# Performance work log

Measured on AMD Instinct MI355X. Metric: run time of the kernel, lower is better.

The kernel has to match this reference:

```python
import jax, jax.numpy as jnp
import numpy as np

N, IN_DIM, OUT_DIM, H = 8192, 128, 128, 2
HD = OUT_DIM // H
NEG_SLOPE = 0.2


def setup_inputs() -> dict:
    key = jax.random.key(0)
    k1, k2, k3, k4, k5 = jax.random.split(key, 5)
    x = jax.random.normal(k1, (N, IN_DIM), dtype=jnp.float32)
    adj = jax.random.randint(k2, (N, N), 0, 2).astype(jnp.float32)
    W = jax.random.normal(k3, (IN_DIM, OUT_DIM), dtype=jnp.float32) / np.sqrt(IN_DIM)
    a_src = jax.random.normal(k4, (H, HD), dtype=jnp.float32) * 0.01
    a_dst = jax.random.normal(k5, (H, HD), dtype=jnp.float32) * 0.01
    return {"x": x, "adj": adj, "W": W, "a_src": a_src, "a_dst": a_dst}


def reference(x, adj, W, a_src, a_dst):
    # h: (N, H, HD)
    h = (x @ W).reshape(N, H, HD)
    # per-node additive score halves: (N, H)
    e_src = jnp.einsum('nhd,hd->nh', h, a_src)
    e_dst = jnp.einsum('nhd,hd->nh', h, a_dst)
    # attn logits: (N_i, N_j, H); torch code adds e_src[i] + e_dst[j]
    logits = jax.nn.leaky_relu(e_src[:, None, :] + e_dst[None, :, :], NEG_SLOPE)
    logits = jnp.where(adj[:, :, None] > 0, logits, -jnp.inf)
    # softmax over neighbor axis j (dim=1), matching F.softmax(attn, dim=1)
    attn = jax.nn.softmax(logits, axis=1)
    # dropout omitted (eval mode)
    out = jnp.einsum('ijh,jhd->ihd', attn, h).reshape(N, OUT_DIM)
    return out
```

## Files before the change

kernel.cpp:

```cpp
#include <hip/hip_runtime.h>
#include <hip/hip_bf16.h>

#define N 8192
#define IND 128
#define OUTD 128
#define JC 8
#define JLEN 1024
#define OSTEPS 8

typedef float f32x4 __attribute__((ext_vector_type(4)));
typedef short s16x8 __attribute__((ext_vector_type(8)));
typedef _Float16 f16;
typedef _Float16 f16x4 __attribute__((ext_vector_type(4)));

static __device__ inline unsigned short f2bf(float f) {
    union { float f; unsigned u; } v; v.f = f;
    unsigned u = v.u + 0x7fffu + ((v.u >> 16) & 1u);
    return (unsigned short)(u >> 16);
}
static __device__ inline float bf2f(unsigned short b) {
    union { unsigned u; float f; } v; v.u = ((unsigned)b) << 16;
    return v.f;
}

__global__ __launch_bounds__(256) void k1_xw(const float* __restrict__ x,
                                             const float* __restrict__ W,
                                             unsigned short* __restrict__ hT) {
    __shared__ unsigned short Wl[128 * 130];
    const int tid = threadIdx.x;
    {
        int k = tid >> 1, n0 = (tid & 1) * 64;
        const float4* src = (const float4*)(W + k * 128 + n0);
#pragma unroll
        for (int v = 0; v < 16; ++v) {
            float4 f = src[v];
            int base = k * 130 + n0 + v * 4;
            Wl[base + 0] = f2bf(f.x);
            Wl[base + 1] = f2bf(f.y);
            Wl[base + 2] = f2bf(f.z);
            Wl[base + 3] = f2bf(f.w);
        }
    }
    __syncthreads();
    const int wave = tid >> 6, lane = tid & 63;
    const int m = lane & 15, quad = lane >> 4;
    const int ibase = blockIdx.x * 64 + wave * 16;
    const int irow = ibase + m;

    f32x4 acc[8];
#pragma unroll
    for (int t = 0; t < 8; ++t) acc[t] = (f32x4){0.f, 0.f, 0.f, 0.f};

#pragma unroll
    for (int ks = 0; ks < 4; ++ks) {
        const int k0 = ks * 32 + quad * 8;
        const float4* xp = (const float4*)(x + (size_t)irow * 128 + k0);
        float4 xa = xp[0], xb = xp[1];
        s16x8 afrag;
        afrag[0] = (short)f2bf(xa.x); afrag[1] = (short)f2bf(xa.y);
        afrag[2] = (short)f2bf(xa.z); afrag[3] = (short)f2bf(xa.w);
        afrag[4] = (short)f2bf(xb.x); afrag[5] = (short)f2bf(xb.y);
        afrag[6] = (short)f2bf(xb.z); afrag[7] = (short)f2bf(xb.w);
#pragma unroll
        for (int nt = 0; nt < 8; ++nt) {
            const int n = nt * 16 + m;
            s16x8 bfrag;
#pragma unroll
            for (int j = 0; j < 8; ++j)
                bfrag[j] = (short)Wl[(k0 + j) * 130 + n];
            acc[nt] = __builtin_amdgcn_mfma_f32_16x16x32_bf16(afrag, bfrag, acc[nt], 0, 0, 0);
        }
    }
#pragma unroll
    for (int nt = 0; nt < 8; ++nt) {
        const int c = nt * 16 + m;
        const int i0 = ibase + quad * 4;
        ushort4 pk;
        pk.x = f2bf(acc[nt][0]); pk.y = f2bf(acc[nt][1]);
        pk.z = f2bf(acc[nt][2]); pk.w = f2bf(acc[nt][3]);
        *(ushort4*)(hT + (size_t)c * N + i0) = pk;
    }
}

__global__ __launch_bounds__(256) void k2_e(const unsigned short* __restrict__ hT,
                                            const float* __restrict__ a_src,
                                            const float* __restrict__ a_dst,
                                            float* __restrict__ As, float* __restrict__ Cs,
                                            float4* __restrict__ BD) {
    const int i = blockIdx.x * 256 + threadIdx.x;
    float es0 = 0.f, ed0 = 0.f, es1 = 0.f, ed1 = 0.f;
#pragma unroll 8
    for (int c = 0; c < 128; ++c) {
        float v = bf2f(hT[(size_t)c * N + i]);
        float as = a_src[c], ad = a_dst[c];
        if (c < 64) { es0 += v * as; ed0 += v * ad; }
        else        { es1 += v * as; ed1 += v * ad; }
    }
    As[i]     = __expf(es0);
    As[N + i] = __expf(es1);
    Cs[i]     = __expf(0.2f * es0);
    Cs[N + i] = __expf(0.2f * es1);
    float4 bd;
    bd.x = __expf(ed0); bd.y = __expf(0.2f * ed0);
    bd.z = __expf(ed1); bd.w = __expf(0.2f * ed1);
    BD[i] = bd;
}

__global__ __launch_bounds__(256, 2) void k3_main(const float* __restrict__ adj,
                                                  const unsigned short* __restrict__ hT,
                                                  const float* __restrict__ As,
                                                  const float* __restrict__ Cs,
                                                  const float4* __restrict__ BD,
                                                  f16* __restrict__ Up,
                                                  float* __restrict__ Lp) {
    __shared__ float4 BDl[JLEN + JLEN / 8];
    const int tid = threadIdx.x;
    const int wave = tid >> 6, lane = tid & 63;
    const int m = lane & 15, quad = lane >> 4;
    const int ibase = blockIdx.y * 64 + wave * 16;
    const int irow = ibase + m;
    const int jc = blockIdx.x;
    const int j0 = jc * JLEN;

    for (int t = tid; t < JLEN; t += 256) BDl[t + (t >> 3)] = BD[j0 + t];

    const float A0 = As[irow], C0 = Cs[irow];
    const float A1 = As[N + irow], C1 = Cs[N + irow];

    f32x4 acc[2][4];
#pragma unroll
    for (int h = 0; h < 2; ++h)
#pragma unroll
        for (int nt = 0; nt < 4; ++nt) acc[h][nt] = (f32x4){0.f, 0.f, 0.f, 0.f};
    float ls0 = 0.f, ls1 = 0.f;

    const float* adjrow = adj + (size_t)irow * N + j0;
    __syncthreads();

    float4 aj[2][8];
#pragma unroll
    for (int kc = 0; kc < 4; ++kc) {
        aj[0][kc * 2]     = *(const float4*)(adjrow + kc * 32 + quad * 8);
        aj[0][kc * 2 + 1] = *(const float4*)(adjrow + kc * 32 + quad * 8 + 4);
    }

#pragma unroll
    for (int os = 0; os < OSTEPS; ++os) {
        const int cur = os & 1, nxt = cur ^ 1;
        const int osn = (os < OSTEPS - 1) ? os + 1 : os;
#pragma unroll
        for (int kc = 0; kc < 4; ++kc) {
            aj[nxt][kc * 2]     = *(const float4*)(adjrow + osn * 128 + kc * 32 + quad * 8);
            aj[nxt][kc * 2 + 1] = *(const float4*)(adjrow + osn * 128 + kc * 32 + quad * 8 + 4);
        }
#pragma unroll
        for (int kc = 0; kc < 4; ++kc) {
            const int jq = j0 + os * 128 + kc * 32 + quad * 8;
            s16x8 h0[4], h1[4];
#pragma unroll
            for (int nt = 0; nt < 4; ++nt) {
                h0[nt] = *(const s16x8*)(hT + (size_t)(nt * 16 + m) * N + jq);
                h1[nt] = *(const s16x8*)(hT + (size_t)(nt * 16 + m + 64) * N + jq);
            }
            float ajv[8];
            *(float4*)(ajv)     = aj[cur][kc * 2];
            *(float4*)(ajv + 4) = aj[cur][kc * 2 + 1];
            const int bb = os * 128 + kc * 32 + quad * 8;
            const int bidx = bb + (bb >> 3);
            s16x8 p0, p1;
#pragma unroll
            for (int jj = 0; jj < 8; ++jj) {
                float4 bd = BDl[bidx + jj];
                float w0 = fmaxf(A0 * bd.x, C0 * bd.y);
                float pv0 = ajv[jj] * w0;
                ls0 += pv0;
                p0[jj] = (short)f2bf(pv0);
                float w1 = fmaxf(A1 * bd.z, C1 * bd.w);
                float pv1 = ajv[jj] * w1;
                ls1 += pv1;
                p1[jj] = (short)f2bf(pv1);
            }
#pragma unroll
            for (int nt = 0; nt < 4; ++nt) {
                acc[0][nt] = __builtin_amdgcn_mfma_f32_16x16x32_bf16(p0, h0[nt], acc[0][nt], 0, 0, 0);
                acc[1][nt] = __builtin_amdgcn_mfma_f32_16x16x32_bf16(p1, h1[nt], acc[1][nt], 0, 0, 0);
            }
        }
    }

    ls0 += __shfl_xor(ls0, 16, 64);
    ls0 += __shfl_xor(ls0, 32, 64);
    ls1 += __shfl_xor(ls1, 16, 64);
    ls1 += __shfl_xor(ls1, 32, 64);

    f16* Ub = Up + (size_t)jc * N * 128;
#pragma unroll
    for (int h = 0; h < 2; ++h)
#pragma unroll
        for (int nt = 0; nt < 4; ++nt) {
            const int c = h * 64 + nt * 16 + m;
            const int ib = ibase + quad * 4;
#pragma unroll
            for (int r = 0; r < 4; ++r)
                Ub[(size_t)(ib + r) * 128 + c] = (f16)acc[h][nt][r];
        }
    if (quad == 0) {
        Lp[((size_t)jc * 2 + 0) * N + irow] = ls0;
        Lp[((size_t)jc * 2 + 1) * N + irow] = ls1;
    }
}

__global__ __launch_bounds__(256) void k4_reduce(const f16* __restrict__ Up,
                                                 const float* __restrict__ Lp,
                                                 float* __restrict__ out) {
    const int base = (blockIdx.x * 256 + threadIdx.x) * 4;
    const int i = base >> 7, c = base & 127, h = c >> 6;
    float su0 = 0.f, su1 = 0.f, su2 = 0.f, su3 = 0.f, sl = 0.f;
#pragma unroll
    for (int jcc = 0; jcc < JC; ++jcc) {
        f16x4 u = *(const f16x4*)(Up + (size_t)jcc * N * 128 + base);
        su0 += (float)u[0]; su1 += (float)u[1];
        su2 += (float)u[2]; su3 += (float)u[3];
        sl += Lp[((size_t)jcc * 2 + h) * N + i];
    }
    float inv = 1.0f / sl;
    float4 o; o.x = su0 * inv; o.y = su1 * inv; o.z = su2 * inv; o.w = su3 * inv;
    *(float4*)(out + base) = o;
}

extern "C" void kernel_launch(void* const* d_in, const int* in_sizes, int n_in,
                              void* d_out, int out_size, void* d_ws, size_t ws_size,
                              hipStream_t stream) {
    const float* x     = (const float*)d_in[0];
    const float* adj   = (const float*)d_in[1];
    const float* W     = (const float*)d_in[2];
    const float* a_src = (const float*)d_in[3];
    const float* a_dst = (const float*)d_in[4];
    float* out = (float*)d_out;
    char* ws = (char*)d_ws;

    size_t off = 0;
    unsigned short* hT = (unsigned short*)(ws + off); off += (size_t)128 * N * 2;
    float* As = (float*)(ws + off); off += (size_t)2 * N * 4;
    float* Cs = (float*)(ws + off); off += (size_t)2 * N * 4;
    float4* BD = (float4*)(ws + off); off += (size_t)N * 16;

    f16* Up = (f16*)(ws + off);
    float* Lp = (float*)(ws + off + (size_t)JC * N * 128 * 2);

    k1_xw<<<N / 64, 256, 0, stream>>>(x, W, hT);
    k2_e<<<N / 256, 256, 0, stream>>>(hT, a_src, a_dst, As, Cs, BD);
    dim3 g3(JC, N / 64);
    k3_main<<<g3, 256, 0, stream>>>(adj, hT, As, Cs, BD, Up, Lp);
    k4_reduce<<<(N * 128) / (256 * 4), 256, 0, stream>>>(Up, Lp, out);
}
```

Before: 511.2 us.

## Pack adjacency into bitmask in a pre-pass and consume bits in main kernel

Adds a pre-pass kernel that ballots the fp32 adjacency matrix into a 64-bit-per-word bitmask. The main attention kernel then reads compact mask words and selects weights instead of streaming 256 MB of fp32 adjacency with double-buffered register prefetch. The change also raises the occupancy hint to 4 blocks per SM and swaps the grid axes so row blocks vary fastest. The full adjacency is still read once by the pack kernel, so the saving comes from dropping the register-heavy prefetch and improving the main kernel's latency hiding, at the cost of an extra launch and an 8 MB bitmask buffer.

After: 514.4 us. About the same (+0.6%).

```diff
diff --git a/kernel.cpp b/kernel.cpp
--- a/kernel.cpp
+++ b/kernel.cpp
@@ -7,6 +7,7 @@
 #define JC 8
 #define JLEN 1024
 #define OSTEPS 8
+#define NW64 (N / 64)
 
 typedef float f32x4 __attribute__((ext_vector_type(4)));
 typedef short s16x8 __attribute__((ext_vector_type(8)));
@@ -21,6 +22,22 @@
 static __device__ inline float bf2f(unsigned short b) {
     union { unsigned u; float f; } v; v.u = ((unsigned)b) << 16;
     return v.f;
+}
+
+__global__ __launch_bounds__(256) void k0_pack(const float* __restrict__ adj,
+                                               unsigned long long* __restrict__ bits) {
+    const int row = blockIdx.x;
+    const int wave = threadIdx.x >> 6, lane = threadIdx.x & 63;
+    const float* src = adj + (size_t)row * N + wave * 2048;
+    unsigned long long acc = 0;
+#pragma unroll 8
+    for (int t = 0; t < 32; ++t) {
+        float v = src[t * 64 + lane];
+        unsigned long long b = __ballot(v != 0.0f);
+        if (lane == t) acc = b;
+    }
+    if (lane < 32)
+        bits[(size_t)row * NW64 + wave * 32 + lane] = acc;
 }
 
 __global__ __launch_bounds__(256) void k1_xw(const float* __restrict__ x,
@@ -106,7 +123,7 @@
     BD[i] = bd;
 }
 
-__global__ __launch_bounds__(256, 2) void k3_main(const float* __restrict__ adj,
+__global__ __launch_bounds__(256, 4) void k3_main(const unsigned long long* __restrict__ bits,
                                                   const unsigned short* __restrict__ hT,
                                                   const float* __restrict__ As,
                                                   const float* __restrict__ Cs,
@@ -117,9 +134,9 @@
     const int tid = threadIdx.x;
     const int wave = tid >> 6, lane = tid & 63;
     const int m = lane & 15, quad = lane >> 4;
-    const int ibase = blockIdx.y * 64 + wave * 16;
+    const int ibase = blockIdx.x * 64 + wave * 16;
     const int irow = ibase + m;
-    const int jc = blockIdx.x;
+    const int jc = blockIdx.y;
     const int j0 = jc * JLEN;
 
     for (int t = tid; t < JLEN; t += 256) BDl[t + (t >> 3)] = BD[j0 + t];
@@ -134,25 +151,14 @@
         for (int nt = 0; nt < 4; ++nt) acc[h][nt] = (f32x4){0.f, 0.f, 0.f, 0.f};
     float ls0 = 0.f, ls1 = 0.f;
 
-    const float* adjrow = adj + (size_t)irow * N + j0;
+    const unsigned long long* mrow = bits + (size_t)irow * NW64 + (j0 >> 6);
+    const int shbase = quad * 8;
     __syncthreads();
 
-    float4 aj[2][8];
-#pragma unroll
-    for (int kc = 0; kc < 4; ++kc) {
-        aj[0][kc * 2]     = *(const float4*)(adjrow + kc * 32 + quad * 8);
-        aj[0][kc * 2 + 1] = *(const float4*)(adjrow + kc * 32 + quad * 8 + 4);
-    }
-
-#pragma unroll
+#pragma unroll 2
     for (int os = 0; os < OSTEPS; ++os) {
-        const int cur = os & 1, nxt = cur ^ 1;
-        const int osn = (os < OSTEPS - 1) ? os + 1 : os;
-#pragma unroll
-        for (int kc = 0; kc < 4; ++kc) {
-            aj[nxt][kc * 2]     = *(const float4*)(adjrow + osn * 128 + kc * 32 + quad * 8);
-            aj[nxt][kc * 2 + 1] = *(const float4*)(adjrow + osn * 128 + kc * 32 + quad * 8 + 4);
-        }
+        const unsigned long long mk0 = mrow[os * 2];
+        const unsigned long long mk1 = mrow[os * 2 + 1];
 #pragma unroll
         for (int kc = 0; kc < 4; ++kc) {
             const int jq = j0 + os * 128 + kc * 32 + quad * 8;
@@ -162,9 +168,9 @@
                 h0[nt] = *(const s16x8*)(hT + (size_t)(nt * 16 + m) * N + jq);
                 h1[nt] = *(const s16x8*)(hT + (size_t)(nt * 16 + m + 64) * N + jq);
             }
-            float ajv[8];
-            *(float4*)(ajv)     = aj[cur][kc * 2];
-            *(float4*)(ajv + 4) = aj[cur][kc * 2 + 1];
+            const unsigned long long mk = (kc < 2) ? mk0 : mk1;
+            const unsigned mbyte = (unsigned)(mk >> ((kc & 1) * 32 + shbase)) & 0xffu;
+
             const int bb = os * 128 + kc * 32 + quad * 8;
             const int bidx = bb + (bb >> 3);
             s16x8 p0, p1;
@@ -172,12 +178,13 @@
             for (int jj = 0; jj < 8; ++jj) {
                 float4 bd = BDl[bidx + jj];
                 float w0 = fmaxf(A0 * bd.x, C0 * bd.y);
-                float pv0 = ajv[jj] * w0;
+                float w1 = fmaxf(A1 * bd.z, C1 * bd.w);
+                bool on = (mbyte >> jj) & 1u;
+                float pv0 = on ? w0 : 0.0f;
+                float pv1 = on ? w1 : 0.0f;
                 ls0 += pv0;
+                ls1 += pv1;
                 p0[jj] = (short)f2bf(pv0);
-                float w1 = fmaxf(A1 * bd.z, C1 * bd.w);
-                float pv1 = ajv[jj] * w1;
-                ls1 += pv1;
                 p1[jj] = (short)f2bf(pv1);
             }
 #pragma unroll
@@ -244,13 +251,15 @@
     float* As = (float*)(ws + off); off += (size_t)2 * N * 4;
     float* Cs = (float*)(ws + off); off += (size_t)2 * N * 4;
     float4* BD = (float4*)(ws + off); off += (size_t)N * 16;
+    unsigned long long* bits = (unsigned long long*)(ws + off); off += (size_t)N * NW64 * 8;
 
     f16* Up = (f16*)(ws + off);
     float* Lp = (float*)(ws + off + (size_t)JC * N * 128 * 2);
 
+    k0_pack<<<N, 256, 0, stream>>>(adj, bits);
     k1_xw<<<N / 64, 256, 0, stream>>>(x, W, hT);
     k2_e<<<N / 256, 256, 0, stream>>>(hT, a_src, a_dst, As, Cs, BD);
-    dim3 g3(JC, N / 64);
-    k3_main<<<g3, 256, 0, stream>>>(adj, hT, As, Cs, BD, Up, Lp);
+    dim3 g3(N / 64, JC);
+    k3_main<<<g3, 256, 0, stream>>>(bits, hT, As, Cs, BD, Up, Lp);
     k4_reduce<<<(N * 128) / (256 * 4), 256, 0, stream>>>(Up, Lp, out);
 }
```
